# Kernel tuning notes

Hardware: AMD Instinct MI355X
Metric: run time of the kernel (lower is better)

The kernel has to match this reference:

```python
import jax, jax.numpy as jnp
import numpy as np

B, S, D_IN, D_OUT = 4, 2048, 4096, 16384


def setup_inputs() -> dict:
    key = jax.random.key(0)
    k1, k2, k3, k4 = jax.random.split(key, 4)
    x = jax.random.normal(k1, (B, S, D_IN), dtype=jnp.float32)
    # per-channel symmetric int8 weights, [out_features, in_features]
    weight_int8 = jax.random.randint(k2, (D_OUT, D_IN), -128, 128, dtype=jnp.int32).astype(jnp.int8)
    # per-channel weight scales (positive, realistic magnitude)
    weight_scale = jax.random.uniform(k3, (D_OUT,), dtype=jnp.float32) * 0.01 + 1e-4
    # static per-tensor activation scale (calibrated constant)
    act_scale = jnp.float32(0.02)
    bias = jax.random.normal(k4, (D_OUT,), dtype=jnp.float32) * 0.1
    return {"x": x, "weight_int8": weight_int8, "weight_scale": weight_scale,
            "act_scale": act_scale, "bias": bias}


def reference(x, weight_int8, weight_scale, act_scale, bias):
    orig_shape = x.shape
    orig_dtype = x.dtype
    x2d = x.reshape(-1, orig_shape[-1])  # [M, D_in]
    # static per-tensor symmetric activation quantization
    x_int8 = jnp.clip(jnp.round(x2d.astype(jnp.float32) / act_scale), -128, 127).astype(jnp.int8)
    y_int32 = jnp.matmul(x_int8, weight_int8.T, preferred_element_type=jnp.int32)  # [M, D_out]
    output_scale = (act_scale * weight_scale).astype(jnp.float32)  # [D_out]
    y = y_int32.astype(jnp.float32) * output_scale[None, :] + bias.astype(jnp.float32)[None, :]
    return y.reshape(*orig_shape[:-1], y.shape[-1]).astype(orig_dtype)
```

## Files before the change

kernel.cpp:

```cpp
#include <hip/hip_runtime.h>
#include <stdint.h>

#define GAS __attribute__((address_space(1)))
#define LAS __attribute__((address_space(3)))

typedef int v4i __attribute__((ext_vector_type(4)));

constexpr int Mdim = 8192;
constexpr int Ndim = 16384;
constexpr int Kdim = 4096;

__device__ __forceinline__ int pack4i8(int a, int b, int c, int d) {
    return (a & 255) | ((b & 255) << 8) | ((c & 255) << 16) | ((d & 255) << 24);
}

__device__ __forceinline__ int qz(float v, float inv) {
    return (int)fminf(fmaxf(rintf(v * inv), -128.0f), 127.0f);
}

__global__ void k_quant_x(const float* __restrict__ x, const float* __restrict__ asc,
                          int8_t* __restrict__ xq) {
    const int i = blockIdx.x * blockDim.x + threadIdx.x;
    const float inv = 1.0f / *asc;
    const float4* xv = (const float4*)x + (size_t)i * 4;
    float4 f0 = xv[0], f1 = xv[1], f2 = xv[2], f3 = xv[3];
    int4 o;
    o.x = pack4i8(qz(f0.x, inv), qz(f0.y, inv), qz(f0.z, inv), qz(f0.w, inv));
    o.y = pack4i8(qz(f1.x, inv), qz(f1.y, inv), qz(f1.z, inv), qz(f1.w, inv));
    o.z = pack4i8(qz(f2.x, inv), qz(f2.y, inv), qz(f2.z, inv), qz(f2.w, inv));
    o.w = pack4i8(qz(f3.x, inv), qz(f3.y, inv), qz(f3.z, inv), qz(f3.w, inv));
    ((int4*)xq)[i] = o;
}

__global__ void k_conv_w(const int* __restrict__ w, int8_t* __restrict__ wq) {
    const int i = blockIdx.x * blockDim.x + threadIdx.x;
    const int4* wv = (const int4*)w + (size_t)i * 4;
    int4 a = wv[0], b = wv[1], c = wv[2], d = wv[3];
    int4 o;
    o.x = pack4i8(a.x, a.y, a.z, a.w);
    o.y = pack4i8(b.x, b.y, b.z, b.w);
    o.z = pack4i8(c.x, c.y, c.z, c.w);
    o.w = pack4i8(d.x, d.y, d.z, d.w);
    ((int4*)wq)[i] = o;
}

constexpr int NSTEP = Kdim / 64;

__global__ __launch_bounds__(256, 2)
void k_gemm_pc(const int8_t* __restrict__ Aq, const int8_t* __restrict__ Bq,
               const float* __restrict__ wscale, const float* __restrict__ asc,
               const float* __restrict__ bias, float* __restrict__ out) {
    __shared__ __align__(16) int8_t lds[49152];
    const int tid = threadIdx.x, lane = tid & 63, w = tid >> 6;
    const int wm = w >> 1, wn = w & 1;
    const int lrow = lane & 15, kgrp = lane >> 4;

    const int bid = blockIdx.x;
    const int swz = ((bid & 7) << 9) | (bid >> 3);
    const int mt = swz & 31, nt = swz >> 5;
    const int m0 = mt << 8, n0 = nt << 7;

    const int srow = (w << 4) + (lane >> 2);
    const int scol = (((lane & 3) ^ ((lane >> 3) & 3)) << 4);
    const int8_t* gA[4];
    const int8_t* gB[2];
#pragma unroll
    for (int u = 0; u < 4; ++u)
        gA[u] = Aq + (size_t)(m0 + u * 64 + srow) * Kdim + scol;
#pragma unroll
    for (int u = 0; u < 2; ++u)
        gB[u] = Bq + (size_t)(n0 + u * 64 + srow) * Kdim + scol;
    const int dstoff = w << 10;

    auto stage = [&](int slot, int kb) {
        int8_t* ba = lds + slot * 24576 + dstoff;
        int8_t* bb = ba + 16384;
#pragma unroll
        for (int u = 0; u < 2; ++u)
            __builtin_amdgcn_global_load_lds((const GAS void*)(gB[u] + kb),
                                             (LAS void*)(bb + u * 4096), 16, 0, 0);
#pragma unroll
        for (int u = 0; u < 4; ++u)
            __builtin_amdgcn_global_load_lds((const GAS void*)(gA[u] + kb),
                                             (LAS void*)(ba + u * 4096), 16, 0, 0);
    };

    const int kc = (kgrp ^ ((lrow >> 1) & 3)) << 4;
    const int arowb = (((wm << 7) + lrow) << 6) + kc;
    const int browb = (((wn << 6) + lrow) << 6) + kc;

    v4i acc[8][4];
#pragma unroll
    for (int i = 0; i < 8; ++i)
#pragma unroll
        for (int j = 0; j < 4; ++j) acc[i][j] = (v4i){0, 0, 0, 0};

    v4i a[8], b[4];

    stage(0, 0);
    int kb = 64;
    for (int s = 0; s < NSTEP; ++s) {
        asm volatile("s_waitcnt vmcnt(0)" ::: "memory");
        __builtin_amdgcn_s_barrier();
        __builtin_amdgcn_sched_barrier(0);
        const int8_t* As_ = lds + (s & 1) * 24576;
        const int8_t* Bs_ = As_ + 16384;
#pragma unroll
        for (int f = 0; f < 4; ++f)
            b[f] = *(const v4i*)(Bs_ + browb + f * 1024);
#pragma unroll
        for (int f = 0; f < 8; ++f)
            a[f] = *(const v4i*)(As_ + arowb + f * 1024);
        if (s < NSTEP - 1) { stage((s + 1) & 1, kb); kb += 64; }
        asm volatile("s_waitcnt lgkmcnt(0)" ::: "memory");
        __builtin_amdgcn_sched_barrier(0);
        __builtin_amdgcn_s_setprio(1);
#pragma unroll
        for (int fi = 0; fi < 8; ++fi)
#pragma unroll
            for (int fj = 0; fj < 4; ++fj)
                acc[fi][fj] = __builtin_amdgcn_mfma_i32_16x16x64_i8(a[fi], b[fj], acc[fi][fj], 0, 0, 0);
        __builtin_amdgcn_s_setprio(0);
    }

    const float ascale = *asc;
#pragma unroll
    for (int fj = 0; fj < 4; ++fj) {
        const int col = n0 + (wn << 6) + fj * 16 + lrow;
        const float sc = ascale * wscale[col];
        const float bb = bias[col];
#pragma unroll
        for (int mi = 0; mi < 8; ++mi) {
            const int r0 = m0 + (wm << 7) + mi * 16 + (kgrp << 2);
            float* o = out + (size_t)r0 * Ndim + col;
#pragma unroll
            for (int q = 0; q < 4; ++q)
                o[(size_t)q * Ndim] = (float)acc[mi][fj][q] * sc + bb;
        }
    }
}

template <bool AQ, bool BQ>
__global__ __launch_bounds__(256)
void k_gemm(const int8_t* __restrict__ Aq, const float* __restrict__ Xf,
            const int8_t* __restrict__ Bq, const int* __restrict__ W32,
            const float* __restrict__ wscale, const float* __restrict__ asc,
            const float* __restrict__ bias, float* __restrict__ out) {
    constexpr int BM = 128, BN = 128, BK = 64;
    constexpr int KT = Kdim / BK;
    __shared__ __align__(16) int8_t As[2][BM * BK];
    __shared__ __align__(16) int8_t Bs[2][BN * BK];

    const int tid  = threadIdx.x;
    const int lane = tid & 63;
    const int wid  = tid >> 6;
    const int wm = wid >> 1, wn = wid & 1;
    const int lrow = lane & 15, kgrp = lane >> 4;

    const int cpx = gridDim.x >> 3;
    const int swz = ((int)blockIdx.x & 7) * cpx + ((int)blockIdx.x >> 3);
    const int mt = swz & (Mdim / BM - 1);
    const int nt = swz / (Mdim / BM);
    const int m0 = mt * BM, n0 = nt * BN;

    const float ascale = *asc;
    const float inv = 1.0f / ascale;

    v4i acc[4][4];
#pragma unroll
    for (int i = 0; i < 4; ++i)
#pragma unroll
        for (int j = 0; j < 4; ++j) acc[i][j] = (v4i){0, 0, 0, 0};

    auto stage = [&](int buf, int kt) {
        const int k0 = kt * BK;
        if constexpr (AQ) {
            int8_t* ldsp = &As[buf][wid << 10];
            const int8_t* g = Aq + (size_t)(m0 + (tid >> 2)) * Kdim + k0 + ((tid & 3) << 4);
            __builtin_amdgcn_global_load_lds((const GAS void*)g, (LAS void*)ldsp, 16, 0, 0);
            __builtin_amdgcn_global_load_lds((const GAS void*)(g + (size_t)64 * Kdim),
                                             (LAS void*)(ldsp + 4096), 16, 0, 0);
        } else {
            const int row = tid >> 1, cb = (tid & 1) << 5;
            const float4* src = (const float4*)(Xf + (size_t)(m0 + row) * Kdim + k0 + cb);
            int t[8];
#pragma unroll
            for (int j = 0; j < 8; ++j) {
                float4 f = src[j];
                t[j] = pack4i8(qz(f.x, inv), qz(f.y, inv), qz(f.z, inv), qz(f.w, inv));
            }
            int4* dst = (int4*)&As[buf][row * BK + cb];
            dst[0] = make_int4(t[0], t[1], t[2], t[3]);
            dst[1] = make_int4(t[4], t[5], t[6], t[7]);
        }
        if constexpr (BQ) {
            int8_t* ldsp = &Bs[buf][wid << 10];
            const int8_t* g = Bq + (size_t)(n0 + (tid >> 2)) * Kdim + k0 + ((tid & 3) << 4);
            __builtin_amdgcn_global_load_lds((const GAS void*)g, (LAS void*)ldsp, 16, 0, 0);
            __builtin_amdgcn_global_load_lds((const GAS void*)(g + (size_t)64 * Kdim),
                                             (LAS void*)(ldsp + 4096), 16, 0, 0);
        } else {
            const int row = tid >> 1, cb = (tid & 1) << 5;
            const int4* src = (const int4*)(W32 + (size_t)(n0 + row) * Kdim + k0 + cb);
            int t[8];
#pragma unroll
            for (int j = 0; j < 8; ++j) {
                int4 vv = src[j];
                t[j] = pack4i8(vv.x, vv.y, vv.z, vv.w);
            }
            int4* dst = (int4*)&Bs[buf][row * BK + cb];
            dst[0] = make_int4(t[0], t[1], t[2], t[3]);
            dst[1] = make_int4(t[4], t[5], t[6], t[7]);
        }
    };

    stage(0, 0);
    for (int kt = 0; kt < KT; ++kt) {
        const int cur = kt & 1;
        __syncthreads();
        if (kt + 1 < KT) stage(cur ^ 1, kt + 1);

        v4i a[4], b[4];
        const int koff = kgrp << 4;
#pragma unroll
        for (int i = 0; i < 4; ++i) {
            a[i] = *(const v4i*)&As[cur][(wm * 64 + i * 16 + lrow) * BK + koff];
            b[i] = *(const v4i*)&Bs[cur][(wn * 64 + i * 16 + lrow) * BK + koff];
        }
#pragma unroll
        for (int i = 0; i < 4; ++i)
#pragma unroll
            for (int j = 0; j < 4; ++j)
                acc[i][j] = __builtin_amdgcn_mfma_i32_16x16x64_i8(a[i], b[j], acc[i][j], 0, 0, 0);
    }

#pragma unroll
    for (int j = 0; j < 4; ++j) {
        const int col = n0 + wn * 64 + j * 16 + lrow;
        const float sc = ascale * wscale[col];
        const float bb = bias[col];
#pragma unroll
        for (int i = 0; i < 4; ++i) {
            const int r0 = m0 + wm * 64 + i * 16 + (kgrp << 2);
            float* o = out + (size_t)r0 * Ndim + col;
#pragma unroll
            for (int r = 0; r < 4; ++r)
                o[(size_t)r * Ndim] = (float)acc[i][j][r] * sc + bb;
        }
    }
}

extern "C" void kernel_launch(void* const* d_in, const int* in_sizes, int n_in,
                              void* d_out, int out_size, void* d_ws, size_t ws_size,
                              hipStream_t stream) {
    const float* x      = (const float*)d_in[0];
    const int*   w32    = (const int*)d_in[1];
    const float* wscale = (const float*)d_in[2];
    const float* asc    = (const float*)d_in[3];
    const float* bias   = (const float*)d_in[4];
    float* out = (float*)d_out;

    const size_t nx = (size_t)Mdim * Kdim;
    const size_t nw = (size_t)Ndim * Kdim;
    int8_t* xq = (int8_t*)d_ws;
    int8_t* wq = xq + nx;

    const bool haveX = ws_size >= nx;
    const bool haveW = ws_size >= nx + nw;

    if (haveX) k_quant_x<<<(int)(nx / 16 / 256), 256, 0, stream>>>(x, asc, xq);
    if (haveW) k_conv_w<<<(int)(nw / 16 / 256), 256, 0, stream>>>(w32, wq);

    if (haveW) {
        dim3 grid((Mdim / 256) * (Ndim / 128));
        k_gemm_pc<<<grid, 256, 0, stream>>>(xq, wq, wscale, asc, bias, out);
    } else if (haveX) {
        dim3 grid((Mdim / 128) * (Ndim / 128));
        k_gemm<true, false><<<grid, 256, 0, stream>>>(xq, x, wq, w32, wscale, asc, bias, out);
    } else {
        dim3 grid((Mdim / 128) * (Ndim / 128));
        k_gemm<false, false><<<grid, 256, 0, stream>>>(xq, x, wq, w32, wscale, asc, bias, out);
    }
}
```

Measured before the change: 936.4 us.

## Restructure int8 GEMM to 128x256 tiles with B loaded directly into registers

Changes the block tile from 256x128 to 128x256, with each wave owning a 64-column slice of N. Only the shared A tile is staged through LDS, using a 4-slot ring with three tiles in flight. Each wave's private B fragments now go straight from global memory into double-buffered registers. This drops the per-step vmcnt(0) wait and halves LDS use, aiming to hide global latency better. The cost is uncoalesced direct B loads and a deep vmcnt dependency; the code also relies on barrier ordering with no explicit wait on the async LDS loads.

Result: no change. 931.9 us (-0.5%).

```diff
diff --git a/kernel.cpp b/kernel.cpp
--- a/kernel.cpp
+++ b/kernel.cpp
@@ -46,48 +46,59 @@
 
 constexpr int NSTEP = Kdim / 64;
 
+#define WINDOW(T, BC, BN, DOLOAD, DOSTAGE)                                   \
+  {                                                                          \
+    __builtin_amdgcn_sched_barrier(0);                                       \
+    __builtin_amdgcn_s_barrier();                                            \
+    __builtin_amdgcn_sched_barrier(0);                                       \
+    if (DOSTAGE) stageA((T) + 3);                                            \
+    if (DOLOAD) {                                                            \
+      _Pragma("unroll") for (int f = 0; f < 4; ++f)                          \
+        BN[f] = *(const v4i*)(pB[f] + (((T) + 1) << 6));                     \
+    }                                                                        \
+    const int8_t* S_ = lds + (((T) & 3) << 13);                              \
+    v4i a_[8];                                                               \
+    _Pragma("unroll") for (int f = 0; f < 8; ++f)                            \
+      a_[f] = *(const v4i*)(S_ + aoff + f * 1024);                           \
+    _Pragma("unroll") for (int fi = 0; fi < 8; ++fi)                         \
+      _Pragma("unroll") for (int fj = 0; fj < 4; ++fj)                       \
+        acc[fi][fj] = __builtin_amdgcn_mfma_i32_16x16x64_i8(                 \
+            a_[fi], BC[fj], acc[fi][fj], 0, 0, 0);                           \
+  }
+
 __global__ __launch_bounds__(256, 2)
-void k_gemm_pc(const int8_t* __restrict__ Aq, const int8_t* __restrict__ Bq,
+void k_gemm_dr(const int8_t* __restrict__ Aq, const int8_t* __restrict__ Bq,
                const float* __restrict__ wscale, const float* __restrict__ asc,
                const float* __restrict__ bias, float* __restrict__ out) {
-    __shared__ __align__(16) int8_t lds[49152];
+    __shared__ __align__(16) int8_t lds[32768];
     const int tid = threadIdx.x, lane = tid & 63, w = tid >> 6;
-    const int wm = w >> 1, wn = w & 1;
     const int lrow = lane & 15, kgrp = lane >> 4;
 
     const int bid = blockIdx.x;
     const int swz = ((bid & 7) << 9) | (bid >> 3);
-    const int mt = swz & 31, nt = swz >> 5;
-    const int m0 = mt << 8, n0 = nt << 7;
-
-    const int srow = (w << 4) + (lane >> 2);
-    const int scol = (((lane & 3) ^ ((lane >> 3) & 3)) << 4);
-    const int8_t* gA[4];
-    const int8_t* gB[2];
-#pragma unroll
-    for (int u = 0; u < 4; ++u)
-        gA[u] = Aq + (size_t)(m0 + u * 64 + srow) * Kdim + scol;
-#pragma unroll
-    for (int u = 0; u < 2; ++u)
-        gB[u] = Bq + (size_t)(n0 + u * 64 + srow) * Kdim + scol;
+    const int mt = swz & 63, nt = swz >> 6;
+    const int m0 = mt << 7, n0 = nt << 8;
+
+    const int srow = tid >> 2;
+    const int scol = (((tid & 3) ^ ((tid >> 3) & 3)) << 4);
+    const int8_t* gA0 = Aq + (size_t)(m0 + srow) * Kdim + scol;
+    const int8_t* gA1 = gA0 + (size_t)64 * Kdim;
     const int dstoff = w << 10;
 
-    auto stage = [&](int slot, int kb) {
-        int8_t* ba = lds + slot * 24576 + dstoff;
-        int8_t* bb = ba + 16384;
-#pragma unroll
-        for (int u = 0; u < 2; ++u)
-            __builtin_amdgcn_global_load_lds((const GAS void*)(gB[u] + kb),
-                                             (LAS void*)(bb + u * 4096), 16, 0, 0);
-#pragma unroll
-        for (int u = 0; u < 4; ++u)
-            __builtin_amdgcn_global_load_lds((const GAS void*)(gA[u] + kb),
-                                             (LAS void*)(ba + u * 4096), 16, 0, 0);
+    auto stageA = [&](int t) {
+        int8_t* d = lds + ((t & 3) << 13) + dstoff;
+        const int kb = t << 6;
+        __builtin_amdgcn_global_load_lds((const GAS void*)(gA0 + kb), (LAS void*)d, 16, 0, 0);
+        __builtin_amdgcn_global_load_lds((const GAS void*)(gA1 + kb), (LAS void*)(d + 4096), 16, 0, 0);
     };
 
+    const int8_t* pB[4];
+#pragma unroll
+    for (int f = 0; f < 4; ++f)
+        pB[f] = Bq + (size_t)(n0 + (w << 6) + f * 16 + lrow) * Kdim + (kgrp << 4);
+
     const int kc = (kgrp ^ ((lrow >> 1) & 3)) << 4;
-    const int arowb = (((wm << 7) + lrow) << 6) + kc;
-    const int browb = (((wn << 6) + lrow) << 6) + kc;
+    const int aoff = lrow * 64 + kc;
 
     v4i acc[8][4];
 #pragma unroll
@@ -95,43 +106,34 @@
 #pragma unroll
         for (int j = 0; j < 4; ++j) acc[i][j] = (v4i){0, 0, 0, 0};
 
-    v4i a[8], b[4];
-
-    stage(0, 0);
-    int kb = 64;
-    for (int s = 0; s < NSTEP; ++s) {
-        asm volatile("s_waitcnt vmcnt(0)" ::: "memory");
-        __builtin_amdgcn_s_barrier();
-        __builtin_amdgcn_sched_barrier(0);
-        const int8_t* As_ = lds + (s & 1) * 24576;
-        const int8_t* Bs_ = As_ + 16384;
-#pragma unroll
-        for (int f = 0; f < 4; ++f)
-            b[f] = *(const v4i*)(Bs_ + browb + f * 1024);
-#pragma unroll
-        for (int f = 0; f < 8; ++f)
-            a[f] = *(const v4i*)(As_ + arowb + f * 1024);
-        if (s < NSTEP - 1) { stage((s + 1) & 1, kb); kb += 64; }
-        asm volatile("s_waitcnt lgkmcnt(0)" ::: "memory");
-        __builtin_amdgcn_sched_barrier(0);
-        __builtin_amdgcn_s_setprio(1);
-#pragma unroll
-        for (int fi = 0; fi < 8; ++fi)
-#pragma unroll
-            for (int fj = 0; fj < 4; ++fj)
-                acc[fi][fj] = __builtin_amdgcn_mfma_i32_16x16x64_i8(a[fi], b[fj], acc[fi][fj], 0, 0, 0);
-        __builtin_amdgcn_s_setprio(0);
-    }
+    v4i bP[4], bQ[4];
+
+    stageA(0); stageA(1); stageA(2);
+#pragma unroll
+    for (int f = 0; f < 4; ++f) bP[f] = *(const v4i*)(pB[f]);
+    asm volatile("s_waitcnt vmcnt(0)" ::: "memory");
+
+    WINDOW(0, bP, bQ, 1, 1)
+    WINDOW(1, bQ, bP, 1, 1)
+    for (int p = 1; p < 30; ++p) {
+        const int t = 2 * p;
+        WINDOW(t,     bP, bQ, 1, 1)
+        WINDOW(t + 1, bQ, bP, 1, 1)
+    }
+    WINDOW(60, bP, bQ, 1, 1)
+    WINDOW(61, bQ, bP, 1, 0)
+    WINDOW(62, bP, bQ, 1, 0)
+    WINDOW(63, bQ, bP, 0, 0)
 
     const float ascale = *asc;
 #pragma unroll
     for (int fj = 0; fj < 4; ++fj) {
-        const int col = n0 + (wn << 6) + fj * 16 + lrow;
+        const int col = n0 + (w << 6) + fj * 16 + lrow;
         const float sc = ascale * wscale[col];
         const float bb = bias[col];
 #pragma unroll
         for (int mi = 0; mi < 8; ++mi) {
-            const int r0 = m0 + (wm << 7) + mi * 16 + (kgrp << 2);
+            const int r0 = m0 + mi * 16 + (kgrp << 2);
             float* o = out + (size_t)r0 * Ndim + col;
 #pragma unroll
             for (int q = 0; q < 4; ++q)
@@ -272,8 +274,8 @@
     if (haveW) k_conv_w<<<(int)(nw / 16 / 256), 256, 0, stream>>>(w32, wq);
 
     if (haveW) {
-        dim3 grid((Mdim / 256) * (Ndim / 128));
-        k_gemm_pc<<<grid, 256, 0, stream>>>(xq, wq, wscale, asc, bias, out);
+        dim3 grid((Mdim / 128) * (Ndim / 256));
+        k_gemm_dr<<<grid, 256, 0, stream>>>(xq, wq, wscale, asc, bias, out);
     } else if (haveX) {
         dim3 grid((Mdim / 128) * (Ndim / 128));
         k_gemm<true, false><<<grid, 256, 0, stream>>>(xq, x, wq, w32, wscale, asc, bias, out);
```

## Pre-pack weights in MFMA fragment order and load B directly to registers

Applied to the files above, without the earlier changes.

The weight conversion kernel now writes int8 weights in a fragment-major layout matching the 16x16x64 MFMA operand, so the GEMM loads B straight from global memory into registers one step ahead instead of staging it through LDS. A is staged through a 4-deep LDS ring (64 KB) with two tiles in flight and partial vmcnt waits, replacing the double buffer that waited for all loads every step. The aim is to cut LDS traffic and barrier stalls and keep more loads overlapping the MFMAs. In exchange, LDS per block grows, which may limit occupancy at two blocks per CU, and B reads now come directly from global memory and cache.

Result: slower. 962.8 us (+2.8%).

```diff
diff --git a/kernel.cpp b/kernel.cpp
--- a/kernel.cpp
+++ b/kernel.cpp
@@ -32,25 +32,53 @@
     ((int4*)xq)[i] = o;
 }
 
-__global__ void k_conv_w(const int* __restrict__ w, int8_t* __restrict__ wq) {
-    const int i = blockIdx.x * blockDim.x + threadIdx.x;
-    const int4* wv = (const int4*)w + (size_t)i * 4;
-    int4 a = wv[0], b = wv[1], c = wv[2], d = wv[3];
+__global__ void k_pack_w(const int* __restrict__ w, int8_t* __restrict__ wp) {
+    const int c = blockIdx.x * blockDim.x + threadIdx.x;
+    const int l = c & 63, ks = (c >> 6) & 63, nt = c >> 12;
+    const int n = nt * 16 + (l & 15);
+    const int k = (ks << 6) + ((l >> 4) << 4);
+    const int4* src = (const int4*)(w + (size_t)n * Kdim + k);
+    int4 a = src[0], b = src[1], cc = src[2], d = src[3];
     int4 o;
     o.x = pack4i8(a.x, a.y, a.z, a.w);
     o.y = pack4i8(b.x, b.y, b.z, b.w);
-    o.z = pack4i8(c.x, c.y, c.z, c.w);
+    o.z = pack4i8(cc.x, cc.y, cc.z, cc.w);
     o.w = pack4i8(d.x, d.y, d.z, d.w);
-    ((int4*)wq)[i] = o;
-}
-
-constexpr int NSTEP = Kdim / 64;
+    ((int4*)wp)[c] = o;
+}
+
+#define VMW(N) asm volatile("s_waitcnt vmcnt(" #N ")" ::: "memory")
+
+#define STEP(T, BC, BN, LB, SA, VMN)                                         \
+  {                                                                          \
+    VMW(VMN);                                                                \
+    __builtin_amdgcn_s_barrier();                                            \
+    __builtin_amdgcn_sched_barrier(0);                                       \
+    if (LB) {                                                                \
+      _Pragma("unroll") for (int f = 0; f < 4; ++f)                          \
+        BN[f] = *(const v4i*)(Bp + ((((size_t)(ntb + f)) << 6 | ((T) + 1))   \
+                                    << 10) + (lane << 4));                   \
+    }                                                                        \
+    if (SA) stA((T) + 2);                                                    \
+    {                                                                        \
+      const int8_t* S_ = lds + (((T) & 3) << 14);                            \
+      v4i a_[8];                                                             \
+      _Pragma("unroll") for (int f = 0; f < 8; ++f)                          \
+        a_[f] = *(const v4i*)(S_ + aoff + f * 1024);                         \
+      __builtin_amdgcn_s_setprio(1);                                         \
+      _Pragma("unroll") for (int fi = 0; fi < 8; ++fi)                       \
+        _Pragma("unroll") for (int fj = 0; fj < 4; ++fj)                     \
+          acc[fi][fj] = __builtin_amdgcn_mfma_i32_16x16x64_i8(               \
+              a_[fi], BC[fj], acc[fi][fj], 0, 0, 0);                         \
+      __builtin_amdgcn_s_setprio(0);                                         \
+    }                                                                        \
+  }
 
 __global__ __launch_bounds__(256, 2)
-void k_gemm_pc(const int8_t* __restrict__ Aq, const int8_t* __restrict__ Bq,
+void k_gemm_bp(const int8_t* __restrict__ Aq, const int8_t* __restrict__ Bp,
                const float* __restrict__ wscale, const float* __restrict__ asc,
                const float* __restrict__ bias, float* __restrict__ out) {
-    __shared__ __align__(16) int8_t lds[49152];
+    __shared__ __align__(16) int8_t lds[65536];
     const int tid = threadIdx.x, lane = tid & 63, w = tid >> 6;
     const int wm = w >> 1, wn = w & 1;
     const int lrow = lane & 15, kgrp = lane >> 4;
@@ -60,34 +88,27 @@
     const int mt = swz & 31, nt = swz >> 5;
     const int m0 = mt << 8, n0 = nt << 7;
 
-    const int srow = (w << 4) + (lane >> 2);
-    const int scol = (((lane & 3) ^ ((lane >> 3) & 3)) << 4);
+    const int srow = tid >> 2;
+    const int scol = (((tid & 3) ^ ((tid >> 3) & 3)) << 4);
     const int8_t* gA[4];
-    const int8_t* gB[2];
 #pragma unroll
     for (int u = 0; u < 4; ++u)
         gA[u] = Aq + (size_t)(m0 + u * 64 + srow) * Kdim + scol;
-#pragma unroll
-    for (int u = 0; u < 2; ++u)
-        gB[u] = Bq + (size_t)(n0 + u * 64 + srow) * Kdim + scol;
     const int dstoff = w << 10;
 
-    auto stage = [&](int slot, int kb) {
-        int8_t* ba = lds + slot * 24576 + dstoff;
-        int8_t* bb = ba + 16384;
-#pragma unroll
-        for (int u = 0; u < 2; ++u)
-            __builtin_amdgcn_global_load_lds((const GAS void*)(gB[u] + kb),
-                                             (LAS void*)(bb + u * 4096), 16, 0, 0);
+    auto stA = [&](int t) {
+        int8_t* base = lds + ((t & 3) << 14) + dstoff;
+        const int kb = t << 6;
 #pragma unroll
         for (int u = 0; u < 4; ++u)
             __builtin_amdgcn_global_load_lds((const GAS void*)(gA[u] + kb),
-                                             (LAS void*)(ba + u * 4096), 16, 0, 0);
+                                             (LAS void*)(base + u * 4096), 16, 0, 0);
     };
 
+    const int ntb = (n0 >> 4) + (wn << 2);
+
     const int kc = (kgrp ^ ((lrow >> 1) & 3)) << 4;
-    const int arowb = (((wm << 7) + lrow) << 6) + kc;
-    const int browb = (((wn << 6) + lrow) << 6) + kc;
+    const int aoff = ((wm << 7) + lrow) * 64 + kc;
 
     v4i acc[8][4];
 #pragma unroll
@@ -95,33 +116,24 @@
 #pragma unroll
         for (int j = 0; j < 4; ++j) acc[i][j] = (v4i){0, 0, 0, 0};
 
-    v4i a[8], b[4];
-
-    stage(0, 0);
-    int kb = 64;
-    for (int s = 0; s < NSTEP; ++s) {
-        asm volatile("s_waitcnt vmcnt(0)" ::: "memory");
-        __builtin_amdgcn_s_barrier();
-        __builtin_amdgcn_sched_barrier(0);
-        const int8_t* As_ = lds + (s & 1) * 24576;
-        const int8_t* Bs_ = As_ + 16384;
-#pragma unroll
-        for (int f = 0; f < 4; ++f)
-            b[f] = *(const v4i*)(Bs_ + browb + f * 1024);
-#pragma unroll
-        for (int f = 0; f < 8; ++f)
-            a[f] = *(const v4i*)(As_ + arowb + f * 1024);
-        if (s < NSTEP - 1) { stage((s + 1) & 1, kb); kb += 64; }
-        asm volatile("s_waitcnt lgkmcnt(0)" ::: "memory");
-        __builtin_amdgcn_sched_barrier(0);
-        __builtin_amdgcn_s_setprio(1);
-#pragma unroll
-        for (int fi = 0; fi < 8; ++fi)
-#pragma unroll
-            for (int fj = 0; fj < 4; ++fj)
-                acc[fi][fj] = __builtin_amdgcn_mfma_i32_16x16x64_i8(a[fi], b[fj], acc[fi][fj], 0, 0, 0);
-        __builtin_amdgcn_s_setprio(0);
-    }
+    v4i bP[4], bQ[4];
+
+    stA(0); stA(1);
+#pragma unroll
+    for (int f = 0; f < 4; ++f)
+        bP[f] = *(const v4i*)(Bp + ((((size_t)(ntb + f)) << 6) << 10) + (lane << 4));
+
+    for (int j = 0; j < 15; ++j) {
+        const int t = j << 2;
+        STEP(t + 0, bP, bQ, 1, 1, 8)
+        STEP(t + 1, bQ, bP, 1, 1, 8)
+        STEP(t + 2, bP, bQ, 1, 1, 8)
+        STEP(t + 3, bQ, bP, 1, 1, 8)
+    }
+    STEP(60, bP, bQ, 1, 1, 8)
+    STEP(61, bQ, bP, 1, 1, 8)
+    STEP(62, bP, bQ, 1, 0, 8)
+    STEP(63, bQ, bP, 0, 0, 4)
 
     const float ascale = *asc;
 #pragma unroll
@@ -140,10 +152,10 @@
     }
 }
 
-template <bool AQ, bool BQ>
+template <bool AQ>
 __global__ __launch_bounds__(256)
 void k_gemm(const int8_t* __restrict__ Aq, const float* __restrict__ Xf,
-            const int8_t* __restrict__ Bq, const int* __restrict__ W32,
+            const int* __restrict__ W32,
             const float* __restrict__ wscale, const float* __restrict__ asc,
             const float* __restrict__ bias, float* __restrict__ out) {
     constexpr int BM = 128, BN = 128, BK = 64;
@@ -193,13 +205,7 @@
             dst[0] = make_int4(t[0], t[1], t[2], t[3]);
             dst[1] = make_int4(t[4], t[5], t[6], t[7]);
         }
-        if constexpr (BQ) {
-            int8_t* ldsp = &Bs[buf][wid << 10];
-            const int8_t* g = Bq + (size_t)(n0 + (tid >> 2)) * Kdim + k0 + ((tid & 3) << 4);
-            __builtin_amdgcn_global_load_lds((const GAS void*)g, (LAS void*)ldsp, 16, 0, 0);
-            __builtin_amdgcn_global_load_lds((const GAS void*)(g + (size_t)64 * Kdim),
-                                             (LAS void*)(ldsp + 4096), 16, 0, 0);
-        } else {
+        {
             const int row = tid >> 1, cb = (tid & 1) << 5;
             const int4* src = (const int4*)(W32 + (size_t)(n0 + row) * Kdim + k0 + cb);
             int t[8];
@@ -263,22 +269,22 @@
     const size_t nx = (size_t)Mdim * Kdim;
     const size_t nw = (size_t)Ndim * Kdim;
     int8_t* xq = (int8_t*)d_ws;
-    int8_t* wq = xq + nx;
+    int8_t* wp = xq + nx;
 
     const bool haveX = ws_size >= nx;
     const bool haveW = ws_size >= nx + nw;
 
     if (haveX) k_quant_x<<<(int)(nx / 16 / 256), 256, 0, stream>>>(x, asc, xq);
-    if (haveW) k_conv_w<<<(int)(nw / 16 / 256), 256, 0, stream>>>(w32, wq);
+    if (haveW) k_pack_w<<<(int)(nw / 16 / 256), 256, 0, stream>>>(w32, wp);
 
     if (haveW) {
         dim3 grid((Mdim / 256) * (Ndim / 128));
-        k_gemm_pc<<<grid, 256, 0, stream>>>(xq, wq, wscale, asc, bias, out);
+        k_gemm_bp<<<grid, 256, 0, stream>>>(xq, wp, wscale, asc, bias, out);
     } else if (haveX) {
         dim3 grid((Mdim / 128) * (Ndim / 128));
-        k_gemm<true, false><<<grid, 256, 0, stream>>>(xq, x, wq, w32, wscale, asc, bias, out);
+        k_gemm<true><<<grid, 256, 0, stream>>>(xq, x, w32, wscale, asc, bias, out);
     } else {
         dim3 grid((Mdim / 128) * (Ndim / 128));
-        k_gemm<false, false><<<grid, 256, 0, stream>>>(xq, x, wq, w32, wscale, asc, bias, out);
-    }
-}
+        k_gemm<false><<<grid, 256, 0, stream>>>(xq, x, w32, wscale, asc, bias, out);
+    }
+}
```

## Split K across wave pairs in GEMM and fuse prep kernels into one launch

Applied to the files above, without the earlier changes.

The GEMM now runs 512-thread blocks in which two wave groups each handle half of the K range on separate double-buffered LDS regions. Their int32 accumulators are combined through LDS before the scale/bias epilogue. The x-quantization and weight-narrowing kernels are merged into a single launch. The aim is more waves in flight to hide load latency and one fewer launch, at the cost of 128KB of LDS per block, which limits occupancy to one block per CU, plus an extra reduction pass.

Result: slower. 1.202 ms (+28.3%).

```diff
diff --git a/kernel.cpp b/kernel.cpp
--- a/kernel.cpp
+++ b/kernel.cpp
@@ -32,27 +32,44 @@
     ((int4*)xq)[i] = o;
 }
 
-__global__ void k_conv_w(const int* __restrict__ w, int8_t* __restrict__ wq) {
-    const int i = blockIdx.x * blockDim.x + threadIdx.x;
-    const int4* wv = (const int4*)w + (size_t)i * 4;
-    int4 a = wv[0], b = wv[1], c = wv[2], d = wv[3];
-    int4 o;
-    o.x = pack4i8(a.x, a.y, a.z, a.w);
-    o.y = pack4i8(b.x, b.y, b.z, b.w);
-    o.z = pack4i8(c.x, c.y, c.z, c.w);
-    o.w = pack4i8(d.x, d.y, d.z, d.w);
-    ((int4*)wq)[i] = o;
-}
-
-constexpr int NSTEP = Kdim / 64;
-
-__global__ __launch_bounds__(256, 2)
-void k_gemm_pc(const int8_t* __restrict__ Aq, const int8_t* __restrict__ Bq,
+constexpr int NQB = (int)((size_t)Mdim * Kdim / 16 / 256);
+constexpr int NWB = (int)((size_t)Ndim * Kdim / 16 / 256);
+
+__global__ void k_prep(const float* __restrict__ x, const int* __restrict__ w,
+                       const float* __restrict__ asc,
+                       int8_t* __restrict__ xq, int8_t* __restrict__ wq) {
+    if (blockIdx.x < NQB) {
+        const int i = blockIdx.x * blockDim.x + threadIdx.x;
+        const float inv = 1.0f / *asc;
+        const float4* xv = (const float4*)x + (size_t)i * 4;
+        float4 f0 = xv[0], f1 = xv[1], f2 = xv[2], f3 = xv[3];
+        int4 o;
+        o.x = pack4i8(qz(f0.x, inv), qz(f0.y, inv), qz(f0.z, inv), qz(f0.w, inv));
+        o.y = pack4i8(qz(f1.x, inv), qz(f1.y, inv), qz(f1.z, inv), qz(f1.w, inv));
+        o.z = pack4i8(qz(f2.x, inv), qz(f2.y, inv), qz(f2.z, inv), qz(f2.w, inv));
+        o.w = pack4i8(qz(f3.x, inv), qz(f3.y, inv), qz(f3.z, inv), qz(f3.w, inv));
+        ((int4*)xq)[i] = o;
+    } else {
+        const int i = (blockIdx.x - NQB) * blockDim.x + threadIdx.x;
+        const int4* wv = (const int4*)w + (size_t)i * 4;
+        int4 a = wv[0], b = wv[1], c = wv[2], d = wv[3];
+        int4 o;
+        o.x = pack4i8(a.x, a.y, a.z, a.w);
+        o.y = pack4i8(b.x, b.y, b.z, b.w);
+        o.z = pack4i8(c.x, c.y, c.z, c.w);
+        o.w = pack4i8(d.x, d.y, d.z, d.w);
+        ((int4*)wq)[i] = o;
+    }
+}
+
+
+__global__ __launch_bounds__(512, 2)
+void k_gemm_ks(const int8_t* __restrict__ Aq, const int8_t* __restrict__ Bq,
                const float* __restrict__ wscale, const float* __restrict__ asc,
                const float* __restrict__ bias, float* __restrict__ out) {
-    __shared__ __align__(16) int8_t lds[49152];
+    __shared__ __align__(16) int8_t lds[131072];
     const int tid = threadIdx.x, lane = tid & 63, w = tid >> 6;
-    const int wm = w >> 1, wn = w & 1;
+    const int wm = w >> 2, wn = (w >> 1) & 1, wsK = w & 1;
     const int lrow = lane & 15, kgrp = lane >> 4;
 
     const int bid = blockIdx.x;
@@ -60,34 +77,23 @@
     const int mt = swz & 31, nt = swz >> 5;
     const int m0 = mt << 8, n0 = nt << 7;
 
-    const int srow = (w << 4) + (lane >> 2);
-    const int scol = (((lane & 3) ^ ((lane >> 3) & 3)) << 4);
-    const int8_t* gA[4];
-    const int8_t* gB[2];
-#pragma unroll
-    for (int u = 0; u < 4; ++u)
-        gA[u] = Aq + (size_t)(m0 + u * 64 + srow) * Kdim + scol;
-#pragma unroll
-    for (int u = 0; u < 2; ++u)
-        gB[u] = Bq + (size_t)(n0 + u * 64 + srow) * Kdim + scol;
+    const int srow = tid >> 2;
+    const int scol = (((tid & 3) ^ ((tid >> 3) & 3)) << 4);
+    const int8_t* gA0 = Aq + (size_t)(m0 + srow) * Kdim + scol;
+    const int8_t* gA1 = gA0 + (size_t)128 * Kdim;
+    const int8_t* gB0 = Bq + (size_t)(n0 + srow) * Kdim + scol;
     const int dstoff = w << 10;
 
-    auto stage = [&](int slot, int kb) {
-        int8_t* ba = lds + slot * 24576 + dstoff;
-        int8_t* bb = ba + 16384;
-#pragma unroll
-        for (int u = 0; u < 2; ++u)
-            __builtin_amdgcn_global_load_lds((const GAS void*)(gB[u] + kb),
-                                             (LAS void*)(bb + u * 4096), 16, 0, 0);
-#pragma unroll
-        for (int u = 0; u < 4; ++u)
-            __builtin_amdgcn_global_load_lds((const GAS void*)(gA[u] + kb),
-                                             (LAS void*)(ba + u * 4096), 16, 0, 0);
+    auto stageSlot = [&](int base, int kb) {
+        __builtin_amdgcn_global_load_lds((const GAS void*)(gA0 + kb),
+                                         (LAS void*)(lds + base + dstoff), 16, 0, 0);
+        __builtin_amdgcn_global_load_lds((const GAS void*)(gA1 + kb),
+                                         (LAS void*)(lds + base + 8192 + dstoff), 16, 0, 0);
+        __builtin_amdgcn_global_load_lds((const GAS void*)(gB0 + kb),
+                                         (LAS void*)(lds + base + 16384 + dstoff), 16, 0, 0);
     };
 
     const int kc = (kgrp ^ ((lrow >> 1) & 3)) << 4;
-    const int arowb = (((wm << 7) + lrow) << 6) + kc;
-    const int browb = (((wn << 6) + lrow) << 6) + kc;
 
     v4i acc[8][4];
 #pragma unroll
@@ -95,47 +101,72 @@
 #pragma unroll
         for (int j = 0; j < 4; ++j) acc[i][j] = (v4i){0, 0, 0, 0};
 
-    v4i a[8], b[4];
-
-    stage(0, 0);
-    int kb = 64;
-    for (int s = 0; s < NSTEP; ++s) {
-        asm volatile("s_waitcnt vmcnt(0)" ::: "memory");
+    stageSlot(0, 0);
+    stageSlot(49152, 32 << 6);
+    stageSlot(24576, 1 << 6);
+    stageSlot(49152 + 24576, 33 << 6);
+    asm volatile("s_waitcnt vmcnt(0)" ::: "memory");
+    __builtin_amdgcn_s_barrier();
+    __builtin_amdgcn_sched_barrier(0);
+
+    for (int p = 0; p < 32; ++p) {
+        const int gbase = wsK * 49152 + (p & 1) * 24576;
+        v4i afr[8], bfr[4];
+#pragma unroll
+        for (int f = 0; f < 8; ++f)
+            afr[f] = *(const v4i*)(lds + gbase + ((wm << 7) + f * 16 + lrow) * 64 + kc);
+#pragma unroll
+        for (int f = 0; f < 4; ++f)
+            bfr[f] = *(const v4i*)(lds + gbase + 16384 + ((wn << 6) + f * 16 + lrow) * 64 + kc);
+        asm volatile("s_waitcnt lgkmcnt(0)" ::: "memory");
+        __builtin_amdgcn_sched_barrier(0);
         __builtin_amdgcn_s_barrier();
         __builtin_amdgcn_sched_barrier(0);
-        const int8_t* As_ = lds + (s & 1) * 24576;
-        const int8_t* Bs_ = As_ + 16384;
-#pragma unroll
-        for (int f = 0; f < 4; ++f)
-            b[f] = *(const v4i*)(Bs_ + browb + f * 1024);
-#pragma unroll
-        for (int f = 0; f < 8; ++f)
-            a[f] = *(const v4i*)(As_ + arowb + f * 1024);
-        if (s < NSTEP - 1) { stage((s + 1) & 1, kb); kb += 64; }
-        asm volatile("s_waitcnt lgkmcnt(0)" ::: "memory");
+        if (p < 30) {
+            const int sb = (p & 1) * 24576;
+            stageSlot(sb, (p + 2) << 6);
+            stageSlot(49152 + sb, (34 + p) << 6);
+            asm volatile("s_waitcnt vmcnt(6)" ::: "memory");
+        } else if (p == 30) {
+            asm volatile("s_waitcnt vmcnt(0)" ::: "memory");
+        }
+        __builtin_amdgcn_s_barrier();
         __builtin_amdgcn_sched_barrier(0);
         __builtin_amdgcn_s_setprio(1);
 #pragma unroll
-        for (int fi = 0; fi < 8; ++fi)
-#pragma unroll
-            for (int fj = 0; fj < 4; ++fj)
-                acc[fi][fj] = __builtin_amdgcn_mfma_i32_16x16x64_i8(a[fi], b[fj], acc[fi][fj], 0, 0, 0);
+        for (int mi = 0; mi < 8; ++mi)
+#pragma unroll
+            for (int nj = 0; nj < 4; ++nj)
+                acc[mi][nj] = __builtin_amdgcn_mfma_i32_16x16x64_i8(
+                    afr[mi], bfr[nj], acc[mi][nj], 0, 0, 0);
         __builtin_amdgcn_s_setprio(0);
     }
 
-    const float ascale = *asc;
-#pragma unroll
-    for (int fj = 0; fj < 4; ++fj) {
-        const int col = n0 + (wn << 6) + fj * 16 + lrow;
-        const float sc = ascale * wscale[col];
-        const float bb = bias[col];
-#pragma unroll
-        for (int mi = 0; mi < 8; ++mi) {
-            const int r0 = m0 + (wm << 7) + mi * 16 + (kgrp << 2);
-            float* o = out + (size_t)r0 * Ndim + col;
-#pragma unroll
-            for (int q = 0; q < 4; ++q)
-                o[(size_t)q * Ndim] = (float)acc[mi][fj][q] * sc + bb;
+    const int pair = w >> 1;
+    if (wsK == 1) {
+#pragma unroll
+        for (int mi = 0; mi < 8; ++mi)
+#pragma unroll
+            for (int nj = 0; nj < 4; ++nj)
+                *(v4i*)(lds + pair * 32768 + (mi * 4 + nj) * 1024 + (lane << 4)) = acc[mi][nj];
+    }
+    __syncthreads();
+    if (wsK == 0) {
+        const float ascale = *asc;
+#pragma unroll
+        for (int nj = 0; nj < 4; ++nj) {
+            const int col = n0 + (wn << 6) + nj * 16 + lrow;
+            const float sc = ascale * wscale[col];
+            const float bb = bias[col];
+#pragma unroll
+            for (int mi = 0; mi < 8; ++mi) {
+                const v4i oth = *(const v4i*)(lds + pair * 32768 + (mi * 4 + nj) * 1024 + (lane << 4));
+                const int r0 = m0 + (wm << 7) + mi * 16 + (kgrp << 2);
+                float* o = out + (size_t)r0 * Ndim + col;
+#pragma unroll
+                for (int q = 0; q < 4; ++q)
+                    o[(size_t)q * Ndim] = (float)(acc[mi][nj][q] + oth[q]) * sc + bb;
+            }
         }
     }
 }
@@ -268,13 +299,12 @@
     const bool haveX = ws_size >= nx;
     const bool haveW = ws_size >= nx + nw;
 
-    if (haveX) k_quant_x<<<(int)(nx / 16 / 256), 256, 0, stream>>>(x, asc, xq);
-    if (haveW) k_conv_w<<<(int)(nw / 16 / 256), 256, 0, stream>>>(w32, wq);
-
     if (haveW) {
+        k_prep<<<NQB + NWB, 256, 0, stream>>>(x, w32, asc, xq, wq);
         dim3 grid((Mdim / 256) * (Ndim / 128));
-        k_gemm_pc<<<grid, 256, 0, stream>>>(xq, wq, wscale, asc, bias, out);
+        k_gemm_ks<<<grid, 512, 0, stream>>>(xq, wq, wscale, asc, bias, out);
     } else if (haveX) {
+        k_quant_x<<<NQB, 256, 0, stream>>>(x, asc, xq);
         dim3 grid((Mdim / 128) * (Ndim / 128));
         k_gemm<true, false><<<grid, 256, 0, stream>>>(xq, x, wq, w32, wscale, asc, bias, out);
     } else {
```
